# Kernel tuning notes

Hardware: AMD Instinct MI355X
Metric: run time of the kernel (lower is better)

## Reference

```python
import jax, jax.numpy as jnp
import numpy as np

G, NPG, EPG = 128, 256, 4096   # graphs, nodes/graph, edges/graph
N, E = G * NPG, G * EPG
IN, H = 64, 64
RATIO = 0.5
K = int(RATIO * EPG)  # edges reserved per graph


def setup_inputs() -> dict:
    key = jax.random.key(0)
    ks = jax.random.split(key, 20)
    x = jax.random.normal(ks[0], (N, IN), dtype=jnp.float32)
    # per-graph random edges (block-diagonal structure, contiguous per graph)
    src = jax.random.randint(ks[1], (G, EPG), 0, NPG)
    dst = jax.random.randint(ks[2], (G, EPG), 0, NPG)
    offs = (jnp.arange(G) * NPG)[:, None]
    edge_index = jnp.stack([(src + offs).reshape(-1), (dst + offs).reshape(-1)]).astype(jnp.int64)
    edge_attr = jax.random.uniform(ks[3], (E,), dtype=jnp.float32)
    batch = jnp.repeat(jnp.arange(G), NPG).astype(jnp.int64)

    def w(k, shape):
        return jax.random.normal(k, shape, dtype=jnp.float32) * 0.1
    return {
        'x': x, 'edge_attr': edge_attr,
        'W11': w(ks[4], (H, IN)), 'b11': w(ks[5], (H,)), 'W12': w(ks[6], (H, IN)),
        'W13': w(ks[7], (H, IN)), 'b13': w(ks[8], (H,)),
        'W21': w(ks[9], (H, H)), 'b21': w(ks[10], (H,)), 'W22': w(ks[11], (H, H)),
        'W23': w(ks[12], (H, H)), 'b23': w(ks[13], (H,)),
        'Wm1': w(ks[14], (4 * H, 2 * H)), 'bm1': w(ks[15], (4 * H,)),
        'Wm2': w(ks[16], (1, 4 * H)), 'bm2': w(ks[17], (1,)),
        'edge_index': edge_index, 'batch': batch,
    }


def leconv(x, row, col, ew, W1, b1, W2, W3, b3):
    # PyG LEConv: out_i = sum_{(j->i)} e_ji * (lin1(x_j) - lin2(x_i)) + lin3(x_i)
    a = x @ W1.T + b1          # lin1 (bias)
    b = x @ W2.T               # lin2 (no bias)
    msg = ew[:, None] * (a[row] - b[col])            # [E, H]
    agg = jax.ops.segment_sum(msg, col, num_segments=x.shape[0])
    return agg + x @ W3.T + b3


def relabel_edges(ei):
    # torch relabel(): map used nodes to compact ids; fixed-shape variant returns
    # the remapped edge_index plus a node-presence mask instead of gathering x.
    present = jnp.zeros((N,), jnp.int32).at[ei.reshape(-1)].set(1)
    nid = jnp.where(present == 1, jnp.cumsum(present) - 1, -1)
    return nid[ei], present


def reference(x, edge_attr, W11, b11, W12, W13, b13, W21, b21, W22, W23, b23,
              Wm1, bm1, Wm2, bm2, edge_index, batch):
    row, col = edge_index[0], edge_index[1]
    h = jax.nn.relu(leconv(x, row, col, edge_attr, W11, b11, W12, W13, b13))
    h = leconv(h, row, col, edge_attr, W21, b21, W22, W23, b23)
    # edge scoring MLP on concat(x[row], x[col])
    edge_rep = jnp.concatenate([h[row], h[col]], axis=-1)       # [E, 2H]
    score = (jax.nn.relu(edge_rep @ Wm1.T + bm1) @ Wm2.T + bm2).reshape(-1)  # [E]
    # per-graph top-k split (graphs are uniform -> static shapes)
    s = score.reshape(G, EPG)
    order = jnp.argsort(-s, axis=1)
    keep, drop = order[:, :K], order[:, K:]
    causal_w = jnp.take_along_axis(s, keep, axis=1).reshape(-1)
    conf_w = -jnp.take_along_axis(s, drop, axis=1).reshape(-1)
    eoffs = (jnp.arange(G) * EPG)[:, None]
    kg = (keep + eoffs).reshape(-1)
    dg = (drop + eoffs).reshape(-1)
    causal_ei = edge_index[:, kg]
    conf_ei = edge_index[:, dg]
    causal_ei_rel, causal_mask = relabel_edges(causal_ei)
    conf_ei_rel, conf_mask = relabel_edges(conf_ei)
    out = jnp.concatenate([score, causal_w, conf_w])            # [2E]
    return out, causal_ei_rel, conf_ei_rel, causal_mask, conf_mask
```

## Files before the change

### kernel.cpp

```cpp
#include <hip/hip_runtime.h>
#include <cstddef>

#define G_    128
#define NPG_  256
#define EPG_  4096
#define NN_   32768
#define EE_   524288
#define KK_   2048
#define GK_   262144

#define O_CW  524288
#define O_DW  786432
#define O_CEI 1048576
#define O_FEI 1572864
#define O_CM  2097152
#define O_DM  2129920

typedef float v4f __attribute__((ext_vector_type(4)));
typedef unsigned long long u64;

struct BiasCfg {
  const float* b[8];
};

__device__ __forceinline__ void cswap(u64& a, u64& b, bool d) {
  u64 hi = a > b ? a : b, lo = a > b ? b : a;
  a = d ? hi : lo;
  b = d ? lo : hi;
}

__device__ __forceinline__ void gemm_wt_body(const float* __restrict__ in, int istride,
                                             const float* __restrict__ WT, int wstride,
                                             const BiasCfg& bc, int ncb,
                                             float* __restrict__ out, int ostride,
                                             int bx, float* xT) {
  const int tid = threadIdx.x;
  const int r0 = bx * 64;
#pragma unroll
  for (int it = 0; it < 16; ++it) {
    int idx = tid + it * 256;
    int rr = idx >> 6, kk = idx & 63;
    xT[kk * 68 + rr] = in[(r0 + rr) * istride + kk];
  }
  __syncthreads();
  const int c4 = (tid & 15) * 4;
  const int r4 = (tid >> 4) * 4;
  for (int cb = 0; cb < ncb; ++cb) {
    const float* wp = WT + cb * 64 + c4;
    const float* bp = bc.b[cb];
    float acc[4][4] = {};
#pragma unroll
    for (int k = 0; k < 64; ++k) {
      float4 xv = *(const float4*)&xT[k * 68 + r4];
      float4 wv = *(const float4*)&wp[(size_t)k * wstride];
      float xr[4] = {xv.x, xv.y, xv.z, xv.w};
      float wc[4] = {wv.x, wv.y, wv.z, wv.w};
#pragma unroll
      for (int a = 0; a < 4; ++a)
#pragma unroll
        for (int b = 0; b < 4; ++b)
          acc[a][b] = fmaf(xr[a], wc[b], acc[a][b]);
    }
    float bx4[4] = {0.f, 0.f, 0.f, 0.f};
    if (bp) {
      float4 bb = *(const float4*)&bp[c4];
      bx4[0] = bb.x; bx4[1] = bb.y; bx4[2] = bb.z; bx4[3] = bb.w;
    }
#pragma unroll
    for (int ri = 0; ri < 4; ++ri) {
      v4f st;
      st.x = acc[ri][0] + bx4[0];
      st.y = acc[ri][1] + bx4[1];
      st.z = acc[ri][2] + bx4[2];
      st.w = acc[ri][3] + bx4[3];
      __builtin_nontemporal_store(st, (v4f*)&out[(r0 + r4 + ri) * ostride + cb * 64 + c4]);
    }
    __syncthreads();
  }
}

__global__ __launch_bounds__(256, 4) void gemm_wt(const float* __restrict__ in, int istride,
                                                  const float* __restrict__ WT, int wstride,
                                                  BiasCfg bc, int ncb,
                                                  float* __restrict__ out, int ostride) {
  __shared__ float xT[64 * 68];
  gemm_wt_body(in, istride, WT, wstride, bc, ncb, out, ostride, blockIdx.x, xT);
}

__global__ __launch_bounds__(256) void prep_kernel(const float* __restrict__ Wm1,
                                                   const float* __restrict__ W11, const float* __restrict__ W12,
                                                   const float* __restrict__ W13,
                                                   const float* __restrict__ W21, const float* __restrict__ W22,
                                                   const float* __restrict__ W23,
                                                   float* __restrict__ WmT, float* __restrict__ W1T,
                                                   float* __restrict__ W2T, int* __restrict__ masks) {
  const int b = blockIdx.x;
  const int tid = threadIdx.x;
  if (b < 64) {
    const int k = b;
#pragma unroll
    for (int t = 0; t < 2; ++t) {
      int j = t * 256 + tid;
      int row = j & 255;
      int koff = (j < 256) ? 0 : 64;
      WmT[k * 512 + j] = Wm1[row * 128 + koff + k];
    }
  } else if (b < 80) {
    const int kb = (b - 64) * 4;
    if (tid < 192) {
      int cb = tid >> 6, c = tid & 63;
      const float* Wsrc = (cb == 0) ? W11 : (cb == 1) ? W12 : W13;
#pragma unroll
      for (int s = 0; s < 4; ++s) {
        int k = kb + s;
        W1T[k * 192 + tid] = Wsrc[c * 64 + k];
      }
    }
  } else if (b < 96) {
    const int kb = (b - 80) * 4;
    if (tid < 192) {
      int cb = tid >> 6, c = tid & 63;
      const float* Wsrc = (cb == 0) ? W21 : (cb == 1) ? W22 : W23;
#pragma unroll
      for (int s = 0; s < 4; ++s) {
        int k = kb + s;
        W2T[k * 192 + tid] = Wsrc[c * 64 + k];
      }
    }
  } else {
    int idx = (b - 96) * 1024 + tid * 4;
    int4 z = {0, 0, 0, 0};
    *(int4*)&masks[idx] = z;
  }
}

__global__ __launch_bounds__(256, 4) void phase1(const float* __restrict__ x, const float* __restrict__ W1T,
                                                 BiasCfg bc, float* __restrict__ buf,
                                                 const int* __restrict__ ei, const float* __restrict__ ea,
                                                 float* __restrict__ MT, float* __restrict__ Wc) {
  __shared__ float xT[64 * 68];
  if (blockIdx.x >= 512) {
    const int e = (blockIdx.x - 512) * 256 + threadIdx.x;
    const int r = ei[e];
    const int c = ei[EE_ + e];
    const int g = e >> 12;
    const int gb = g << 8;
    const float w = ea[e];
    atomicAdd(&MT[((size_t)g << 16) + ((size_t)(r - gb) << 8) + (c - gb)], w);
    atomicAdd(&Wc[c], w);
    return;
  }
  gemm_wt_body(x, 64, W1T, 192, bc, 3, buf, 192, blockIdx.x, xT);
}

__global__ __launch_bounds__(256) void mm_agg(const float* __restrict__ MT, const float* __restrict__ buf,
                                              const float* __restrict__ Wc, float* __restrict__ hout,
                                              int do_relu) {
  __shared__ float Ms[64 * 72];
  __shared__ float As[64 * 72];
  const int tid = threadIdx.x;
  const int g = blockIdx.x >> 2;
  const int c0 = (blockIdx.x & 3) * 64;
  const int gbase = g * NPG_;
  const size_t mbase = (size_t)g << 16;
  const int c4 = (tid >> 4) * 4;
  const int k4 = (tid & 15) * 4;
  float acc[4][4] = {};
  for (int kc = 0; kc < 4; ++kc) {
#pragma unroll
    for (int it = 0; it < 16; ++it) {
      int idx = tid + it * 256;
      int rr = idx >> 6, cc = idx & 63;
      Ms[rr * 72 + cc] = MT[mbase + (size_t)(kc * 64 + rr) * 256 + c0 + cc];
      As[rr * 72 + cc] = buf[(gbase + kc * 64 + rr) * 192 + cc];
    }
    __syncthreads();
#pragma unroll
    for (int r = 0; r < 64; ++r) {
      float4 mv = *(const float4*)&Ms[r * 72 + c4];
      float4 av = *(const float4*)&As[r * 72 + k4];
      float mr[4] = {mv.x, mv.y, mv.z, mv.w};
      float ak[4] = {av.x, av.y, av.z, av.w};
#pragma unroll
      for (int ci = 0; ci < 4; ++ci)
#pragma unroll
        for (int ki = 0; ki < 4; ++ki)
          acc[ci][ki] = fmaf(mr[ci], ak[ki], acc[ci][ki]);
    }
    __syncthreads();
  }
#pragma unroll
  for (int ci = 0; ci < 4; ++ci) {
    int n = gbase + c0 + c4 + ci;
    float wcn = Wc[n];
    float4 b4 = *(const float4*)&buf[n * 192 + 64 + k4];
    float4 cc4 = *(const float4*)&buf[n * 192 + 128 + k4];
    float4 st;
    st.x = acc[ci][0] - wcn * b4.x + cc4.x;
    st.y = acc[ci][1] - wcn * b4.y + cc4.y;
    st.z = acc[ci][2] - wcn * b4.z + cc4.z;
    st.w = acc[ci][3] - wcn * b4.w + cc4.w;
    if (do_relu) {
      st.x = fmaxf(st.x, 0.f); st.y = fmaxf(st.y, 0.f);
      st.z = fmaxf(st.z, 0.f); st.w = fmaxf(st.w, 0.f);
    }
    *(float4*)&hout[n * 64 + k4] = st;
  }
}

__global__ __launch_bounds__(256, 4) void score_v4(const float* __restrict__ pq, const int* __restrict__ ei,
                                                   const float* __restrict__ wm2, const float* __restrict__ bm2,
                                                   float* __restrict__ out) {
  __shared__ float Ps[256 * 20];
  __shared__ float Qs[256 * 20];
  const int tid = threadIdx.x;
  const int g = blockIdx.x & 127;
  const int quarter = blockIdx.x >> 7;
  const int gbase = g * NPG_;
  const int ebase = g * EPG_ + quarter * 1024;
  int rl[4], cl[4];
  float acc[4] = {};
#pragma unroll
  for (int j = 0; j < 4; ++j) {
    int e = ebase + j * 256 + tid;
    rl[j] = (ei[e] - gbase) * 20;
    cl[j] = (ei[EE_ + e] - gbase) * 20;
  }
  for (int t = 0; t < 16; ++t) {
    __syncthreads();
#pragma unroll
    for (int it = 0; it < 4; ++it) {
      int idx = tid + it * 256;
      int node = idx >> 2, k4 = (idx & 3) * 4;
      const float* src = &pq[(size_t)(gbase + node) * 512 + t * 16 + k4];
      *(float4*)&Ps[node * 20 + k4] = *(const float4*)src;
      *(float4*)&Qs[node * 20 + k4] = *(const float4*)(src + 256);
    }
    __syncthreads();
#pragma unroll
    for (int k4 = 0; k4 < 16; k4 += 4) {
      float4 w4 = *(const float4*)&wm2[t * 16 + k4];
#pragma unroll
      for (int j = 0; j < 4; ++j) {
        float4 p = *(const float4*)&Ps[rl[j] + k4];
        float4 q = *(const float4*)&Qs[cl[j] + k4];
        acc[j] = fmaf(w4.x, fmaxf(p.x + q.x, 0.f), acc[j]);
        acc[j] = fmaf(w4.y, fmaxf(p.y + q.y, 0.f), acc[j]);
        acc[j] = fmaf(w4.z, fmaxf(p.z + q.z, 0.f), acc[j]);
        acc[j] = fmaf(w4.w, fmaxf(p.w + q.w, 0.f), acc[j]);
      }
    }
  }
  const float beta = bm2[0];
#pragma unroll
  for (int j = 0; j < 4; ++j) out[ebase + j * 256 + tid] = acc[j] + beta;
}

__global__ __launch_bounds__(1024) void sort_kernel(float* __restrict__ out, const int* __restrict__ ei,
                                                    int* __restrict__ kg, int* __restrict__ dg,
                                                    int* __restrict__ cmask, int* __restrict__ dmask) {
  __shared__ u64 keys[EPG_];
  const int g = blockIdx.x;
  const int tid = threadIdx.x;
  const int b = 4 * tid;
  u64 e[4];
  {
    float4 s4 = *(const float4*)&out[g * EPG_ + b];
    float sv[4] = {s4.x, s4.y, s4.z, s4.w};
#pragma unroll
    for (int s = 0; s < 4; ++s) {
      unsigned u = __float_as_uint(sv[s]);
      u = (u & 0x80000000u) ? ~u : (u | 0x80000000u);
      e[s] = ((u64)u << 32) | (unsigned)(~(b + s));
    }
  }
  cswap(e[0], e[1], true);
  cswap(e[2], e[3], false);
  {
    bool d = ((b & 4) == 0);
    cswap(e[0], e[2], d); cswap(e[1], e[3], d);
    cswap(e[0], e[1], d); cswap(e[2], e[3], d);
  }
  for (int k = 8; k <= EPG_; k <<= 1) {
    if (k >= 512) {
#pragma unroll
      for (int s = 0; s < 4; ++s) keys[b + s] = e[s];
      __syncthreads();
      for (int j = k >> 1; j >= 256; j >>= 1) {
        const int jm1 = j - 1;
        const int p0 = tid, p1 = tid + 1024;
        const int i0 = ((p0 & ~jm1) << 1) | (p0 & jm1);
        const int i1 = ((p1 & ~jm1) << 1) | (p1 & jm1);
        u64 a0 = keys[i0], b0 = keys[i0 + j];
        u64 a1 = keys[i1], b1 = keys[i1 + j];
        bool d0 = ((i0 & k) == 0), d1 = ((i1 & k) == 0);
        u64 hi0 = a0 > b0 ? a0 : b0, lo0 = a0 > b0 ? b0 : a0;
        u64 hi1 = a1 > b1 ? a1 : b1, lo1 = a1 > b1 ? b1 : a1;
        keys[i0]     = d0 ? hi0 : lo0;
        keys[i0 + j] = d0 ? lo0 : hi0;
        keys[i1]     = d1 ? hi1 : lo1;
        keys[i1 + j] = d1 ? lo1 : hi1;
        __syncthreads();
      }
#pragma unroll
      for (int s = 0; s < 4; ++s) e[s] = keys[b + s];
    }
    const bool d = ((tid & (k >> 2)) == 0);
    for (int j = (k >> 1) > 128 ? 128 : (k >> 1); j >= 4; j >>= 1) {
      const int delta = j >> 2;
      const bool lower = ((tid & delta) == 0);
      const bool keepmax = (lower == d);
#pragma unroll
      for (int s = 0; s < 4; ++s) {
        u64 p = __shfl_xor(e[s], delta);
        u64 mx = e[s] > p ? e[s] : p;
        u64 mn = e[s] > p ? p : e[s];
        e[s] = keepmax ? mx : mn;
      }
    }
    cswap(e[0], e[2], d); cswap(e[1], e[3], d);
    cswap(e[0], e[1], d); cswap(e[2], e[3], d);
  }
#pragma unroll
  for (int s = 0; s < 4; ++s) {
    const int p = b + s;
    u64 kv = e[s];
    int i = (int)(~(unsigned)kv);
    unsigned hi = (unsigned)(kv >> 32);
    unsigned ub = (hi & 0x80000000u) ? (hi ^ 0x80000000u) : ~hi;
    float sc = __uint_as_float(ub);
    int ed = g * EPG_ + i;
    int r = ei[ed], c = ei[EE_ + ed];
    if (p < KK_) {
      out[O_CW + g * KK_ + p] = sc;
      kg[g * KK_ + p] = ed;
      cmask[r] = 1; cmask[c] = 1;
    } else {
      int q = p - KK_;
      out[O_DW + g * KK_ + q] = -sc;
      dg[g * KK_ + q] = ed;
      dmask[r] = 1; dmask[c] = 1;
    }
  }
}

__global__ __launch_bounds__(1024) void scan_kernel(const int* __restrict__ masks, int* __restrict__ nids) {
  const int which = blockIdx.x;
  const int* m = masks + which * NN_;
  int* nid = nids + which * NN_;
  const int tid = threadIdx.x;
  const int base = tid * 32;
  int local[32];
  int sum = 0;
#pragma unroll
  for (int j = 0; j < 32; ++j) { local[j] = m[base + j]; sum += local[j]; }
  __shared__ int ps[1024];
  ps[tid] = sum;
  __syncthreads();
  for (int off = 1; off < 1024; off <<= 1) {
    int v = (tid >= off) ? ps[tid - off] : 0;
    __syncthreads();
    ps[tid] += v;
    __syncthreads();
  }
  int run = ps[tid] - sum;
#pragma unroll
  for (int j = 0; j < 32; ++j) { run += local[j]; nid[base + j] = run - 1; }
}

__global__ __launch_bounds__(256) void finalize_kernel(const int* __restrict__ kg, const int* __restrict__ dg,
                                                       const int* __restrict__ ei,
                                                       const int* __restrict__ nid_c, const int* __restrict__ nid_d,
                                                       const int* __restrict__ cmask, const int* __restrict__ dmask,
                                                       float* __restrict__ out) {
  const int p = blockIdx.x * 256 + threadIdx.x;
  int e = kg[p];
  out[O_CEI + p]       = (float)nid_c[ei[e]];
  out[O_CEI + GK_ + p] = (float)nid_c[ei[EE_ + e]];
  int e2 = dg[p];
  out[O_FEI + p]       = (float)nid_d[ei[e2]];
  out[O_FEI + GK_ + p] = (float)nid_d[ei[EE_ + e2]];
  if (p < NN_) {
    out[O_CM + p] = (float)cmask[p];
    out[O_DM + p] = (float)dmask[p];
  }
}

extern "C" void kernel_launch(void* const* d_in, const int* in_sizes, int n_in,
                              void* d_out, int out_size, void* d_ws, size_t ws_size,
                              hipStream_t stream) {
  (void)in_sizes; (void)n_in; (void)out_size; (void)ws_size;
  const float* x   = (const float*)d_in[0];
  const float* ea  = (const float*)d_in[1];
  const float* W11 = (const float*)d_in[2];
  const float* b11 = (const float*)d_in[3];
  const float* W12 = (const float*)d_in[4];
  const float* W13 = (const float*)d_in[5];
  const float* b13 = (const float*)d_in[6];
  const float* W21 = (const float*)d_in[7];
  const float* b21 = (const float*)d_in[8];
  const float* W22 = (const float*)d_in[9];
  const float* W23 = (const float*)d_in[10];
  const float* b23 = (const float*)d_in[11];
  const float* Wm1 = (const float*)d_in[12];
  const float* bm1 = (const float*)d_in[13];
  const float* Wm2 = (const float*)d_in[14];
  const float* bm2 = (const float*)d_in[15];
  const int*   ei  = (const int*)d_in[16];
  float* out = (float*)d_out;
  float* ws  = (float*)d_ws;

  float* MT  = ws;
  float* Wc  = ws + 8388608;
  float* buf = ws + 8421376;
  float* pq  = ws;
  float* h_c = ws + 16777216;
  int* kg    = (int*)(ws + 18874368);
  int* dg    = kg + GK_;
  int* cmask = dg + GK_;
  int* dmask = cmask + NN_;
  int* nid_c = dmask + NN_;
  int* nid_d = nid_c + NN_;
  float* WmT = ws + 18874368;
  float* W1T = WmT + 32768;
  float* W2T = W1T + 12288;

  (void)hipMemsetAsync(MT, 0, (size_t)(8388608 + 32768) * sizeof(float), stream);

  prep_kernel<<<160, 256, 0, stream>>>(Wm1, W11, W12, W13, W21, W22, W23, WmT, W1T, W2T, cmask);

  BiasCfg bc1{};
  bc1.b[0] = b11; bc1.b[1] = nullptr; bc1.b[2] = b13;
  phase1<<<2560, 256, 0, stream>>>(x, W1T, bc1, buf, ei, ea, MT, Wc);

  mm_agg<<<512, 256, 0, stream>>>(MT, buf, Wc, h_c, 1);

  BiasCfg bc2{};
  bc2.b[0] = b21; bc2.b[1] = nullptr; bc2.b[2] = b23;
  gemm_wt<<<512, 256, 0, stream>>>(h_c, 64, W2T, 192, bc2, 3, buf, 192);

  mm_agg<<<512, 256, 0, stream>>>(MT, buf, Wc, h_c, 0);

  BiasCfg bc3{};
  for (int cb = 0; cb < 4; ++cb) { bc3.b[cb] = bm1 + cb * 64; bc3.b[cb + 4] = nullptr; }
  gemm_wt<<<512, 256, 0, stream>>>(h_c, 64, WmT, 512, bc3, 8, pq, 512);

  score_v4<<<512, 256, 0, stream>>>(pq, ei, Wm2, bm2, out);

  sort_kernel<<<G_, 1024, 0, stream>>>(out, ei, kg, dg, cmask, dmask);

  scan_kernel<<<2, 1024, 0, stream>>>(cmask, nid_c);

  finalize_kernel<<<GK_ / 256, 256, 0, stream>>>(kg, dg, ei, nid_c, nid_d, cmask, dmask, out);
}
```

Baseline: 360.0 us.

## Build per-graph dense adjacency in shared memory instead of global atomics

Replaces the 32 MB memset plus global atomicAdd scatter into the dense per-graph edge-weight matrix with a kernel that builds half a graph's 256x128 slice in LDS using shared atomics. It then writes the slice out with float4 stores and computes the column sums directly. The fused phase1 kernel is split, so the first linear layer now runs as a separate gemm_wt launch. The goal is to remove the global memset traffic and the contended global atomics. In exchange, each block needs 128 KB of LDS, which limits occupancy, and every block reads all of its graph's edges twice across the two column halves.

```diff
diff --git a/kernel.cpp b/kernel.cpp
--- a/kernel.cpp
+++ b/kernel.cpp
@@ -134,23 +134,38 @@
   }
 }
 
-__global__ __launch_bounds__(256, 4) void phase1(const float* __restrict__ x, const float* __restrict__ W1T,
-                                                 BiasCfg bc, float* __restrict__ buf,
-                                                 const int* __restrict__ ei, const float* __restrict__ ea,
-                                                 float* __restrict__ MT, float* __restrict__ Wc) {
-  __shared__ float xT[64 * 68];
-  if (blockIdx.x >= 512) {
-    const int e = (blockIdx.x - 512) * 256 + threadIdx.x;
-    const int r = ei[e];
-    const int c = ei[EE_ + e];
-    const int g = e >> 12;
-    const int gb = g << 8;
-    const float w = ea[e];
-    atomicAdd(&MT[((size_t)g << 16) + ((size_t)(r - gb) << 8) + (c - gb)], w);
-    atomicAdd(&Wc[c], w);
-    return;
-  }
-  gemm_wt_body(x, 64, W1T, 192, bc, 3, buf, 192, blockIdx.x, xT);
+__global__ __launch_bounds__(256) void build_dense(const int* __restrict__ ei, const float* __restrict__ ea,
+                                                   float* __restrict__ MT, float* __restrict__ Wc) {
+  __shared__ float acc[NPG_ * 128];
+  const int tid = threadIdx.x;
+  const int g = blockIdx.x >> 1;
+  const int c0 = (blockIdx.x & 1) * 128;
+  const int gbase = g * NPG_;
+  const size_t mbase = (size_t)g << 16;
+  for (int i = tid * 4; i < NPG_ * 128; i += 1024) {
+    float4 z = {0.f, 0.f, 0.f, 0.f};
+    *(float4*)&acc[i] = z;
+  }
+  __syncthreads();
+  const int ebase = g * EPG_;
+#pragma unroll
+  for (int it = 0; it < 16; ++it) {
+    int e = ebase + it * 256 + tid;
+    int r = ei[e] - gbase;
+    int ch = ei[EE_ + e] - gbase - c0;
+    float w = ea[e];
+    if ((unsigned)ch < 128u) atomicAdd(&acc[r * 128 + ch], w);
+  }
+  __syncthreads();
+  for (int i = tid; i < NPG_ * 32; i += 256) {
+    int r = i >> 5, c4 = (i & 31) * 4;
+    *(float4*)&MT[mbase + (size_t)r * 256 + c0 + c4] = *(const float4*)&acc[r * 128 + c4];
+  }
+  if (tid < 128) {
+    float s = 0.f;
+    for (int r = 0; r < NPG_; ++r) s += acc[r * 128 + tid];
+    Wc[gbase + c0 + tid] = s;
+  }
 }
 
 __global__ __launch_bounds__(256) void mm_agg(const float* __restrict__ MT, const float* __restrict__ buf,
@@ -425,13 +440,13 @@
   float* W1T = WmT + 32768;
   float* W2T = W1T + 12288;
 
-  (void)hipMemsetAsync(MT, 0, (size_t)(8388608 + 32768) * sizeof(float), stream);
-
   prep_kernel<<<160, 256, 0, stream>>>(Wm1, W11, W12, W13, W21, W22, W23, WmT, W1T, W2T, cmask);
+
+  build_dense<<<256, 256, 0, stream>>>(ei, ea, MT, Wc);
 
   BiasCfg bc1{};
   bc1.b[0] = b11; bc1.b[1] = nullptr; bc1.b[2] = b13;
-  phase1<<<2560, 256, 0, stream>>>(x, W1T, bc1, buf, ei, ea, MT, Wc);
+  gemm_wt<<<512, 256, 0, stream>>>(x, 64, W1T, 192, bc1, 3, buf, 192);
 
   mm_agg<<<512, 256, 0, stream>>>(MT, buf, Wc, h_c, 1);
 
```

Result: faster. 329.1 us (-8.6%).
